# Performance work log

Measured on AMD Instinct MI355X. Metric: run time of the kernel, lower is better.

The kernel has to match this reference:

```python
import jax, jax.numpy as jnp
import numpy as np

D_MODEL = 768
CODEBOOK_SIZE = 2048
CODEBOOK_DIM = 64


def setup_inputs() -> dict:
    key = jax.random.key(0)
    ks = jax.random.split(key, 10)
    B, N = 16, 4096
    h = CODEBOOK_DIM * 2  # 128
    def lin_init(k, fan_in, shape):
        bound = 1.0 / np.sqrt(fan_in)
        return jax.random.uniform(k, shape, jnp.float32, -bound, bound)
    inp = {
        "x": jax.random.normal(ks[0], (B, N, D_MODEL), jnp.float32),
        # encoder: Linear(d_model -> 2*cd), GELU, Linear(2*cd -> cd)
        "enc_w1": lin_init(ks[1], D_MODEL, (D_MODEL, h)),
        "enc_b1": lin_init(ks[2], D_MODEL, (h,)),
        "enc_w2": lin_init(ks[3], h, (h, CODEBOOK_DIM)),
        "enc_b2": lin_init(ks[4], h, (CODEBOOK_DIM,)),
        # codebook: uniform(-1/K, 1/K)
        "codebook": jax.random.uniform(ks[5], (CODEBOOK_SIZE, CODEBOOK_DIM), jnp.float32,
                                        -1.0 / CODEBOOK_SIZE, 1.0 / CODEBOOK_SIZE),
        # decoder: Linear(cd -> 2*cd), GELU, Linear(2*cd -> d_model)
        "dec_w1": lin_init(ks[6], CODEBOOK_DIM, (CODEBOOK_DIM, h)),
        "dec_b1": lin_init(ks[7], CODEBOOK_DIM, (h,)),
        "dec_w2": lin_init(ks[8], h, (h, D_MODEL)),
        "dec_b2": lin_init(ks[9], h, (D_MODEL,)),
    }
    return inp


def reference(x, enc_w1, enc_b1, enc_w2, enc_b2, codebook, dec_w1, dec_b1, dec_w2, dec_b2):
    B, N, _ = x.shape
    # encoder MLP (exact GELU, matching torch default)
    z = jax.nn.gelu(x @ enc_w1 + enc_b1, approximate=False) @ enc_w2 + enc_b2  # (B,N,cd)
    # quantize: squared-distance argmin over codebook
    flat_z = z.reshape(-1, CODEBOOK_DIM)  # (BN, cd)
    dist = (jnp.sum(flat_z * flat_z, axis=1, keepdims=True)
            + jnp.sum(codebook * codebook, axis=1)[None, :]
            - 2.0 * flat_z @ codebook.T)  # (BN, K)
    indices = jnp.argmin(dist, axis=-1)  # (BN,)
    z_q = codebook[indices].reshape(B, N, CODEBOOK_DIM)
    codebook_loss = jnp.mean((jax.lax.stop_gradient(z_q) - z) ** 2)
    embedding_loss = jnp.mean((z_q - jax.lax.stop_gradient(z)) ** 2)
    vq_loss = codebook_loss + 0.25 * embedding_loss
    # straight-through estimator
    z_q = z + jax.lax.stop_gradient(z_q - z)
    # decoder MLP
    x_rec = jax.nn.gelu(z_q @ dec_w1 + dec_b1, approximate=False) @ dec_w2 + dec_b2
    return x_rec, indices.reshape(B, N), vq_loss
```

## Files before the change

### kernel.cpp

```cpp
#include <hip/hip_runtime.h>
#include <math.h>

#define TOKENS 65536
#define DMODEL 768
#define HDIM 128
#define CDIM 64
#define NCODE 2048

__device__ __forceinline__ float gelu_exact(float v) {
    return 0.5f * v * (1.0f + erff(v * 0.7071067811865476f));
}

__global__ __launch_bounds__(256)
void enc_fused(const float* __restrict__ x, const float* __restrict__ w1,
               const float* __restrict__ b1, const float* __restrict__ w2,
               const float* __restrict__ b2, float* __restrict__ Z)
{
    __shared__ union {
        struct { float Xs[64][32]; float Ws[32][128]; } pa;
        struct { float W2s[128][64]; } pb;
    } u;
    __shared__ float H1s[64][132];

    const int t = threadIdx.x;
    const size_t tok0 = (size_t)blockIdx.x * 64;

    const int tg = t >> 5;
    const int cg = t & 31;

    float acc[8][4];
    #pragma unroll
    for (int i = 0; i < 8; ++i)
        #pragma unroll
        for (int j = 0; j < 4; ++j) acc[i][j] = 0.f;

    const int ltok = t >> 2, lkg = t & 3;

    float4 xr0, xr1, wr[4];
    {
        const float4* src = reinterpret_cast<const float4*>(
            x + (tok0 + ltok) * DMODEL + lkg * 8);
        xr0 = src[0]; xr1 = src[1];
        #pragma unroll
        for (int i = 0; i < 4; ++i) {
            int f = t + i * 256;
            int row = f >> 5, c4 = f & 31;
            wr[i] = *reinterpret_cast<const float4*>(w1 + (size_t)row * HDIM + c4 * 4);
        }
    }

    for (int k0 = 0; k0 < DMODEL; k0 += 32) {
        {
            float4* dst = reinterpret_cast<float4*>(&u.pa.Xs[ltok][lkg * 8]);
            dst[0] = xr0; dst[1] = xr1;
            #pragma unroll
            for (int i = 0; i < 4; ++i) {
                int f = t + i * 256;
                int row = f >> 5, c4 = f & 31;
                *reinterpret_cast<float4*>(&u.pa.Ws[row][c4 * 4]) = wr[i];
            }
        }
        __syncthreads();
        if (k0 + 32 < DMODEL) {
            const float4* src = reinterpret_cast<const float4*>(
                x + (tok0 + ltok) * DMODEL + (k0 + 32) + lkg * 8);
            xr0 = src[0]; xr1 = src[1];
            #pragma unroll
            for (int i = 0; i < 4; ++i) {
                int f = t + i * 256;
                int row = f >> 5, c4 = f & 31;
                wr[i] = *reinterpret_cast<const float4*>(
                    w1 + (size_t)(k0 + 32 + row) * HDIM + c4 * 4);
            }
        }
        #pragma unroll
        for (int kk = 0; kk < 32; kk += 4) {
            float4 av[8];
            #pragma unroll
            for (int i = 0; i < 8; ++i)
                av[i] = *reinterpret_cast<const float4*>(&u.pa.Xs[tg * 8 + i][kk]);
            float4 bv[4];
            #pragma unroll
            for (int q = 0; q < 4; ++q)
                bv[q] = *reinterpret_cast<const float4*>(&u.pa.Ws[kk + q][cg * 4]);
            #pragma unroll
            for (int i = 0; i < 8; ++i) {
                acc[i][0] = fmaf(av[i].x, bv[0].x, acc[i][0]);
                acc[i][1] = fmaf(av[i].x, bv[0].y, acc[i][1]);
                acc[i][2] = fmaf(av[i].x, bv[0].z, acc[i][2]);
                acc[i][3] = fmaf(av[i].x, bv[0].w, acc[i][3]);
                acc[i][0] = fmaf(av[i].y, bv[1].x, acc[i][0]);
                acc[i][1] = fmaf(av[i].y, bv[1].y, acc[i][1]);
                acc[i][2] = fmaf(av[i].y, bv[1].z, acc[i][2]);
                acc[i][3] = fmaf(av[i].y, bv[1].w, acc[i][3]);
                acc[i][0] = fmaf(av[i].z, bv[2].x, acc[i][0]);
                acc[i][1] = fmaf(av[i].z, bv[2].y, acc[i][1]);
                acc[i][2] = fmaf(av[i].z, bv[2].z, acc[i][2]);
                acc[i][3] = fmaf(av[i].z, bv[2].w, acc[i][3]);
                acc[i][0] = fmaf(av[i].w, bv[3].x, acc[i][0]);
                acc[i][1] = fmaf(av[i].w, bv[3].y, acc[i][1]);
                acc[i][2] = fmaf(av[i].w, bv[3].z, acc[i][2]);
                acc[i][3] = fmaf(av[i].w, bv[3].w, acc[i][3]);
            }
        }
        __syncthreads();
    }
    {
        float4 b1v = *reinterpret_cast<const float4*>(b1 + cg * 4);
        #pragma unroll
        for (int i = 0; i < 8; ++i) {
            float4 h;
            h.x = gelu_exact(acc[i][0] + b1v.x);
            h.y = gelu_exact(acc[i][1] + b1v.y);
            h.z = gelu_exact(acc[i][2] + b1v.z);
            h.w = gelu_exact(acc[i][3] + b1v.w);
            *reinterpret_cast<float4*>(&H1s[tg * 8 + i][cg * 4]) = h;
        }
    }
    #pragma unroll
    for (int i = 0; i < 8; ++i) {
        int f = t + i * 256;
        int row = f >> 4, c4 = f & 15;
        *reinterpret_cast<float4*>(&u.pb.W2s[row][c4 * 4]) =
            *reinterpret_cast<const float4*>(w2 + (size_t)row * CDIM + c4 * 4);
    }
    __syncthreads();
    const int tg2 = t >> 4;
    const int cg2 = t & 15;
    float accB[4][4];
    #pragma unroll
    for (int i = 0; i < 4; ++i)
        #pragma unroll
        for (int j = 0; j < 4; ++j) accB[i][j] = 0.f;
    #pragma unroll
    for (int k = 0; k < HDIM; k += 4) {
        float4 av[4];
        #pragma unroll
        for (int i = 0; i < 4; ++i)
            av[i] = *reinterpret_cast<const float4*>(&H1s[tg2 * 4 + i][k]);
        float4 bv[4];
        #pragma unroll
        for (int q = 0; q < 4; ++q)
            bv[q] = *reinterpret_cast<const float4*>(&u.pb.W2s[k + q][cg2 * 4]);
        #pragma unroll
        for (int i = 0; i < 4; ++i) {
            accB[i][0] = fmaf(av[i].x, bv[0].x, accB[i][0]);
            accB[i][1] = fmaf(av[i].x, bv[0].y, accB[i][1]);
            accB[i][2] = fmaf(av[i].x, bv[0].z, accB[i][2]);
            accB[i][3] = fmaf(av[i].x, bv[0].w, accB[i][3]);
            accB[i][0] = fmaf(av[i].y, bv[1].x, accB[i][0]);
            accB[i][1] = fmaf(av[i].y, bv[1].y, accB[i][1]);
            accB[i][2] = fmaf(av[i].y, bv[1].z, accB[i][2]);
            accB[i][3] = fmaf(av[i].y, bv[1].w, accB[i][3]);
            accB[i][0] = fmaf(av[i].z, bv[2].x, accB[i][0]);
            accB[i][1] = fmaf(av[i].z, bv[2].y, accB[i][1]);
            accB[i][2] = fmaf(av[i].z, bv[2].z, accB[i][2]);
            accB[i][3] = fmaf(av[i].z, bv[2].w, accB[i][3]);
            accB[i][0] = fmaf(av[i].w, bv[3].x, accB[i][0]);
            accB[i][1] = fmaf(av[i].w, bv[3].y, accB[i][1]);
            accB[i][2] = fmaf(av[i].w, bv[3].z, accB[i][2]);
            accB[i][3] = fmaf(av[i].w, bv[3].w, accB[i][3]);
        }
    }
    {
        float4 b2v = *reinterpret_cast<const float4*>(b2 + cg2 * 4);
        #pragma unroll
        for (int i = 0; i < 4; ++i) {
            float4 o;
            o.x = accB[i][0] + b2v.x;
            o.y = accB[i][1] + b2v.y;
            o.z = accB[i][2] + b2v.z;
            o.w = accB[i][3] + b2v.w;
            *reinterpret_cast<float4*>(Z + (tok0 + tg2 * 4 + i) * CDIM + cg2 * 4) = o;
        }
    }
}

__global__ __launch_bounds__(256)
void vq_kernel(const float* __restrict__ Z, const float* __restrict__ cb,
               const float* __restrict__ cnorm, int* __restrict__ idx_out,
               float* __restrict__ idxf_out, float* __restrict__ loss_accum)
{
    __shared__ float Zs[64][64];
    __shared__ float CsT[64][128];
    __shared__ float tgsum[8];

    const int t = threadIdx.x;
    const size_t tok0 = (size_t)blockIdx.x * 64;
    const int tg = t >> 5, cg = t & 31;
    const int lc = t >> 1, lh = t & 1;

    {
        int ltok = t >> 2, lq = t & 3;
        const float4* src = reinterpret_cast<const float4*>(Z + (tok0 + ltok) * CDIM + lq * 16);
        float4* dst = reinterpret_cast<float4*>(&Zs[ltok][lq * 16]);
        dst[0] = src[0]; dst[1] = src[1]; dst[2] = src[2]; dst[3] = src[3];
    }
    float4 cv[8];
    {
        const float4* src = reinterpret_cast<const float4*>(cb + (size_t)lc * CDIM + lh * 32);
        #pragma unroll
        for (int i = 0; i < 8; ++i) cv[i] = src[i];
    }
    __syncthreads();

    float zn[8];
    {
        #pragma unroll
        for (int i = 0; i < 8; ++i) {
            float a = Zs[tg * 8 + i][cg * 2];
            float b = Zs[tg * 8 + i][cg * 2 + 1];
            zn[i] = fmaf(a, a, b * b);
        }
        #pragma unroll
        for (int m = 16; m >= 1; m >>= 1)
            #pragma unroll
            for (int i = 0; i < 8; ++i) zn[i] += __shfl_xor(zn[i], m, 32);
    }

    float minv[8]; int mini[8];
    #pragma unroll
    for (int i = 0; i < 8; ++i) { minv[i] = INFINITY; mini[i] = 0; }

    for (int tile = 0; tile < 16; ++tile) {
        const int code0 = tile * 128;
        __syncthreads();
        #pragma unroll
        for (int i = 0; i < 8; ++i) {
            int k = lh * 32 + i * 4;
            CsT[k + 0][lc] = cv[i].x;
            CsT[k + 1][lc] = cv[i].y;
            CsT[k + 2][lc] = cv[i].z;
            CsT[k + 3][lc] = cv[i].w;
        }
        __syncthreads();
        if (tile + 1 < 16) {
            const float4* src = reinterpret_cast<const float4*>(
                cb + (size_t)(code0 + 128 + lc) * CDIM + lh * 32);
            #pragma unroll
            for (int i = 0; i < 8; ++i) cv[i] = src[i];
        }

        float dot[8][4];
        #pragma unroll
        for (int i = 0; i < 8; ++i)
            #pragma unroll
            for (int j = 0; j < 4; ++j) dot[i][j] = 0.f;

        #pragma unroll
        for (int k = 0; k < CDIM; k += 4) {
            float4 av[8];
            #pragma unroll
            for (int i = 0; i < 8; ++i)
                av[i] = *reinterpret_cast<const float4*>(&Zs[tg * 8 + i][k]);
            float4 bv[4];
            #pragma unroll
            for (int q = 0; q < 4; ++q)
                bv[q] = *reinterpret_cast<const float4*>(&CsT[k + q][cg * 4]);
            #pragma unroll
            for (int i = 0; i < 8; ++i) {
                dot[i][0] = fmaf(av[i].x, bv[0].x, dot[i][0]);
                dot[i][1] = fmaf(av[i].x, bv[0].y, dot[i][1]);
                dot[i][2] = fmaf(av[i].x, bv[0].z, dot[i][2]);
                dot[i][3] = fmaf(av[i].x, bv[0].w, dot[i][3]);
                dot[i][0] = fmaf(av[i].y, bv[1].x, dot[i][0]);
                dot[i][1] = fmaf(av[i].y, bv[1].y, dot[i][1]);
                dot[i][2] = fmaf(av[i].y, bv[1].z, dot[i][2]);
                dot[i][3] = fmaf(av[i].y, bv[1].w, dot[i][3]);
                dot[i][0] = fmaf(av[i].z, bv[2].x, dot[i][0]);
                dot[i][1] = fmaf(av[i].z, bv[2].y, dot[i][1]);
                dot[i][2] = fmaf(av[i].z, bv[2].z, dot[i][2]);
                dot[i][3] = fmaf(av[i].z, bv[2].w, dot[i][3]);
                dot[i][0] = fmaf(av[i].w, bv[3].x, dot[i][0]);
                dot[i][1] = fmaf(av[i].w, bv[3].y, dot[i][1]);
                dot[i][2] = fmaf(av[i].w, bv[3].z, dot[i][2]);
                dot[i][3] = fmaf(av[i].w, bv[3].w, dot[i][3]);
            }
        }
        #pragma unroll
        for (int j = 0; j < 4; ++j) {
            int ci = code0 + cg * 4 + j;
            float cn = cnorm[ci];
            #pragma unroll
            for (int i = 0; i < 8; ++i) {
                float s = (zn[i] + cn) - 2.f * dot[i][j];
                if (s < minv[i]) { minv[i] = s; mini[i] = ci; }
            }
        }
    }

    #pragma unroll
    for (int i = 0; i < 8; ++i) {
        float v = minv[i]; int ci = mini[i];
        #pragma unroll
        for (int m = 16; m >= 1; m >>= 1) {
            float ov = __shfl_xor(v, m, 32);
            int oi = __shfl_xor(ci, m, 32);
            if (ov < v || (ov == v && oi < ci)) { v = ov; ci = oi; }
        }
        minv[i] = v; mini[i] = ci;
    }

    if (cg == 0) {
        float s = 0.f;
        #pragma unroll
        for (int i = 0; i < 8; ++i) {
            size_t tok = tok0 + tg * 8 + i;
            idx_out[tok] = mini[i];
            idxf_out[tok] = (float)mini[i];
            s += minv[i];
        }
        tgsum[tg] = s;
    }
    __syncthreads();
    if (t == 0) {
        float s = 0.f;
        #pragma unroll
        for (int i = 0; i < 8; ++i) s += tgsum[i];
        atomicAdd(loss_accum, s);
    }
}

__global__ __launch_bounds__(256)
void dec1_kernel(const float* __restrict__ cb, const float* __restrict__ w1,
                 const float* __restrict__ b1, float* __restrict__ T1,
                 float* __restrict__ cnorm)
{
    __shared__ float Cs[64][64];
    __shared__ float Ws[64][128];

    const int t = threadIdx.x;
    const int c0 = blockIdx.x * 64;
    {
        int lc = t >> 2, lq = t & 3;
        const float4* src = reinterpret_cast<const float4*>(cb + (size_t)(c0 + lc) * CDIM + lq * 16);
        float4* dst = reinterpret_cast<float4*>(&Cs[lc][lq * 16]);
        dst[0] = src[0]; dst[1] = src[1]; dst[2] = src[2]; dst[3] = src[3];
    }
    #pragma unroll
    for (int i = 0; i < 8; ++i) {
        int f = t + i * 256;
        int row = f >> 5, c4 = f & 31;
        *reinterpret_cast<float4*>(&Ws[row][c4 * 4]) =
            *reinterpret_cast<const float4*>(w1 + (size_t)row * HDIM + c4 * 4);
    }
    if (t < 64) {
        const float4* p = reinterpret_cast<const float4*>(cb + (size_t)(c0 + t) * CDIM);
        float s = 0.f;
        #pragma unroll
        for (int i = 0; i < 16; ++i) {
            float4 v = p[i];
            s = fmaf(v.x, v.x, s); s = fmaf(v.y, v.y, s);
            s = fmaf(v.z, v.z, s); s = fmaf(v.w, v.w, s);
        }
        cnorm[c0 + t] = s;
    }
    __syncthreads();
    const int tg = t >> 5, cg = t & 31;
    float acc[8][4];
    #pragma unroll
    for (int i = 0; i < 8; ++i)
        #pragma unroll
        for (int j = 0; j < 4; ++j) acc[i][j] = 0.f;
    #pragma unroll
    for (int k = 0; k < CDIM; k += 4) {
        float4 av[8];
        #pragma unroll
        for (int i = 0; i < 8; ++i)
            av[i] = *reinterpret_cast<const float4*>(&Cs[tg * 8 + i][k]);
        float4 bv[4];
        #pragma unroll
        for (int q = 0; q < 4; ++q)
            bv[q] = *reinterpret_cast<const float4*>(&Ws[k + q][cg * 4]);
        #pragma unroll
        for (int i = 0; i < 8; ++i) {
            acc[i][0] = fmaf(av[i].x, bv[0].x, acc[i][0]);
            acc[i][1] = fmaf(av[i].x, bv[0].y, acc[i][1]);
            acc[i][2] = fmaf(av[i].x, bv[0].z, acc[i][2]);
            acc[i][3] = fmaf(av[i].x, bv[0].w, acc[i][3]);
            acc[i][0] = fmaf(av[i].y, bv[1].x, acc[i][0]);
            acc[i][1] = fmaf(av[i].y, bv[1].y, acc[i][1]);
            acc[i][2] = fmaf(av[i].y, bv[1].z, acc[i][2]);
            acc[i][3] = fmaf(av[i].y, bv[1].w, acc[i][3]);
            acc[i][0] = fmaf(av[i].z, bv[2].x, acc[i][0]);
            acc[i][1] = fmaf(av[i].z, bv[2].y, acc[i][1]);
            acc[i][2] = fmaf(av[i].z, bv[2].z, acc[i][2]);
            acc[i][3] = fmaf(av[i].z, bv[2].w, acc[i][3]);
            acc[i][0] = fmaf(av[i].w, bv[3].x, acc[i][0]);
            acc[i][1] = fmaf(av[i].w, bv[3].y, acc[i][1]);
            acc[i][2] = fmaf(av[i].w, bv[3].z, acc[i][2]);
            acc[i][3] = fmaf(av[i].w, bv[3].w, acc[i][3]);
        }
    }
    float4 b1v = *reinterpret_cast<const float4*>(b1 + cg * 4);
    #pragma unroll
    for (int i = 0; i < 8; ++i) {
        float4 h;
        h.x = gelu_exact(acc[i][0] + b1v.x);
        h.y = gelu_exact(acc[i][1] + b1v.y);
        h.z = gelu_exact(acc[i][2] + b1v.z);
        h.w = gelu_exact(acc[i][3] + b1v.w);
        *reinterpret_cast<float4*>(T1 + (size_t)(c0 + tg * 8 + i) * HDIM + cg * 4) = h;
    }
}

__global__ __launch_bounds__(256)
void dec2_kernel(const float* __restrict__ T1, const float* __restrict__ w2,
                 const float* __restrict__ b2, float* __restrict__ table)
{
    __shared__ float As[64][32];
    __shared__ float Ws[32][128];
    const int t = threadIdx.x;
    const int r0 = blockIdx.x * 64;
    const int col0 = blockIdx.y * 128;
    const int tg = t >> 5, cg = t & 31;
    float acc[8][4];
    #pragma unroll
    for (int i = 0; i < 8; ++i)
        #pragma unroll
        for (int j = 0; j < 4; ++j) acc[i][j] = 0.f;

    for (int k0 = 0; k0 < HDIM; k0 += 32) {
        __syncthreads();
        {
            int lr = t >> 2, lk = t & 3;
            const float4* src = reinterpret_cast<const float4*>(T1 + (size_t)(r0 + lr) * HDIM + k0 + lk * 8);
            float4 v0 = src[0], v1 = src[1];
            float4* dst = reinterpret_cast<float4*>(&As[lr][lk * 8]);
            dst[0] = v0; dst[1] = v1;
        }
        #pragma unroll
        for (int i = 0; i < 4; ++i) {
            int f = t + i * 256;
            int row = f >> 5, c4 = f & 31;
            *reinterpret_cast<float4*>(&Ws[row][c4 * 4]) =
                *reinterpret_cast<const float4*>(w2 + (size_t)(k0 + row) * DMODEL + col0 + c4 * 4);
        }
        __syncthreads();
        #pragma unroll
        for (int kk = 0; kk < 32; kk += 4) {
            float4 av[8];
            #pragma unroll
            for (int i = 0; i < 8; ++i)
                av[i] = *reinterpret_cast<const float4*>(&As[tg * 8 + i][kk]);
            float4 bv[4];
            #pragma unroll
            for (int q = 0; q < 4; ++q)
                bv[q] = *reinterpret_cast<const float4*>(&Ws[kk + q][cg * 4]);
            #pragma unroll
            for (int i = 0; i < 8; ++i) {
                acc[i][0] = fmaf(av[i].x, bv[0].x, acc[i][0]);
                acc[i][1] = fmaf(av[i].x, bv[0].y, acc[i][1]);
                acc[i][2] = fmaf(av[i].x, bv[0].z, acc[i][2]);
                acc[i][3] = fmaf(av[i].x, bv[0].w, acc[i][3]);
                acc[i][0] = fmaf(av[i].y, bv[1].x, acc[i][0]);
                acc[i][1] = fmaf(av[i].y, bv[1].y, acc[i][1]);
                acc[i][2] = fmaf(av[i].y, bv[1].z, acc[i][2]);
                acc[i][3] = fmaf(av[i].y, bv[1].w, acc[i][3]);
                acc[i][0] = fmaf(av[i].z, bv[2].x, acc[i][0]);
                acc[i][1] = fmaf(av[i].z, bv[2].y, acc[i][1]);
                acc[i][2] = fmaf(av[i].z, bv[2].z, acc[i][2]);
                acc[i][3] = fmaf(av[i].z, bv[2].w, acc[i][3]);
                acc[i][0] = fmaf(av[i].w, bv[3].x, acc[i][0]);
                acc[i][1] = fmaf(av[i].w, bv[3].y, acc[i][1]);
                acc[i][2] = fmaf(av[i].w, bv[3].z, acc[i][2]);
                acc[i][3] = fmaf(av[i].w, bv[3].w, acc[i][3]);
            }
        }
    }
    float4 b2v = *reinterpret_cast<const float4*>(b2 + col0 + cg * 4);
    #pragma unroll
    for (int i = 0; i < 8; ++i) {
        float4 o;
        o.x = acc[i][0] + b2v.x;
        o.y = acc[i][1] + b2v.y;
        o.z = acc[i][2] + b2v.z;
        o.w = acc[i][3] + b2v.w;
        *reinterpret_cast<float4*>(table + (size_t)(r0 + tg * 8 + i) * DMODEL + col0 + cg * 4) = o;
    }
}

__global__ void gather_kernel(const float* __restrict__ table,
                              const int* __restrict__ idx, float* __restrict__ out,
                              const float* __restrict__ loss_accum,
                              float* __restrict__ loss_out)
{
    if (blockIdx.x == 0 && threadIdx.x == 0) {
        loss_out[0] = loss_accum[0] * (1.25f / 4194304.0f);
    }
    const int F = TOKENS * (DMODEL / 4);
    const float4* tab4 = reinterpret_cast<const float4*>(table);
    float4* out4 = reinterpret_cast<float4*>(out);
    for (int f = blockIdx.x * blockDim.x + threadIdx.x; f < F;
         f += gridDim.x * blockDim.x) {
        int token = f / 192;
        int j = f - token * 192;
        out4[f] = tab4[(size_t)idx[token] * 192 + j];
    }
}

extern "C" void kernel_launch(void* const* d_in, const int* in_sizes, int n_in,
                              void* d_out, int out_size, void* d_ws, size_t ws_size,
                              hipStream_t stream)
{
    const float* x      = (const float*)d_in[0];
    const float* enc_w1 = (const float*)d_in[1];
    const float* enc_b1 = (const float*)d_in[2];
    const float* enc_w2 = (const float*)d_in[3];
    const float* enc_b2 = (const float*)d_in[4];
    const float* cb     = (const float*)d_in[5];
    const float* dec_w1 = (const float*)d_in[6];
    const float* dec_b1 = (const float*)d_in[7];
    const float* dec_w2 = (const float*)d_in[8];
    const float* dec_b2 = (const float*)d_in[9];

    float* out     = (float*)d_out;
    float* xrec    = out;
    float* idxf    = out + (size_t)TOKENS * DMODEL;
    float* lossout = idxf + TOKENS;

    float* ws    = (float*)d_ws;
    float* Z     = ws;
    float* T1    = Z + (size_t)TOKENS * CDIM;
    float* table = T1 + (size_t)NCODE * HDIM;
    float* cnorm = table + (size_t)NCODE * DMODEL;
    int*   idx   = (int*)(cnorm + NCODE);
    float* lacc  = (float*)(idx + TOKENS);

    hipMemsetAsync(lacc, 0, sizeof(float), stream);

    enc_fused<<<TOKENS / 64, 256, 0, stream>>>(x, enc_w1, enc_b1, enc_w2, enc_b2, Z);
    dec1_kernel<<<NCODE / 64, 256, 0, stream>>>(cb, dec_w1, dec_b1, T1, cnorm);
    dec2_kernel<<<dim3(NCODE / 64, DMODEL / 128), 256, 0, stream>>>(T1, dec_w2, dec_b2, table);
    vq_kernel<<<TOKENS / 64, 256, 0, stream>>>(Z, cb, cnorm, idx, idxf, lacc);
    gather_kernel<<<2048, 256, 0, stream>>>(table, idx, xrec, lacc, lossout);
}
```

Before: 949.3 us.

## Pad shared tiles, interleave row mapping, and cut encoder LDS footprint

Shared-memory tiles across the encoder, VQ, and decoder kernels are padded (row strides 36/68) and thread-to-row mapping changes from contiguous (tg*8+i) to strided (tg+8*i), to reduce LDS bank conflicts on the float4 A-operand reads. The encoder's second GEMM now reads w2 directly from global memory with register double-buffering instead of staging it in LDS. H1s is folded into the union, shrinking LDS use, and launch_bounds asks for 4 blocks per CU to raise occupancy. The risks are extra global/L2 traffic for w2 and register pressure from the occupancy hint.

New measurement: 928.4 us. 1.02x faster.

```diff
diff --git a/kernel.cpp b/kernel.cpp
--- a/kernel.cpp
+++ b/kernel.cpp
@@ -11,20 +11,18 @@
     return 0.5f * v * (1.0f + erff(v * 0.7071067811865476f));
 }
 
-__global__ __launch_bounds__(256)
+__global__ __launch_bounds__(256, 4)
 void enc_fused(const float* __restrict__ x, const float* __restrict__ w1,
                const float* __restrict__ b1, const float* __restrict__ w2,
                const float* __restrict__ b2, float* __restrict__ Z)
 {
     __shared__ union {
-        struct { float Xs[64][32]; float Ws[32][128]; } pa;
-        struct { float W2s[128][64]; } pb;
+        struct { float Xs[64][36]; float Ws[32][128]; } a;
+        float H1s[64][132];
     } u;
-    __shared__ float H1s[64][132];
 
     const int t = threadIdx.x;
     const size_t tok0 = (size_t)blockIdx.x * 64;
-
     const int tg = t >> 5;
     const int cg = t & 31;
 
@@ -35,11 +33,11 @@
         for (int j = 0; j < 4; ++j) acc[i][j] = 0.f;
 
     const int ltok = t >> 2, lkg = t & 3;
+    const float* xrow = x + (tok0 + ltok) * DMODEL + lkg * 8;
 
     float4 xr0, xr1, wr[4];
     {
-        const float4* src = reinterpret_cast<const float4*>(
-            x + (tok0 + ltok) * DMODEL + lkg * 8);
+        const float4* src = reinterpret_cast<const float4*>(xrow);
         xr0 = src[0]; xr1 = src[1];
         #pragma unroll
         for (int i = 0; i < 4; ++i) {
@@ -51,19 +49,18 @@
 
     for (int k0 = 0; k0 < DMODEL; k0 += 32) {
         {
-            float4* dst = reinterpret_cast<float4*>(&u.pa.Xs[ltok][lkg * 8]);
+            float4* dst = reinterpret_cast<float4*>(&u.a.Xs[ltok][lkg * 8]);
             dst[0] = xr0; dst[1] = xr1;
             #pragma unroll
             for (int i = 0; i < 4; ++i) {
                 int f = t + i * 256;
                 int row = f >> 5, c4 = f & 31;
-                *reinterpret_cast<float4*>(&u.pa.Ws[row][c4 * 4]) = wr[i];
+                *reinterpret_cast<float4*>(&u.a.Ws[row][c4 * 4]) = wr[i];
             }
         }
         __syncthreads();
         if (k0 + 32 < DMODEL) {
-            const float4* src = reinterpret_cast<const float4*>(
-                x + (tok0 + ltok) * DMODEL + (k0 + 32) + lkg * 8);
+            const float4* src = reinterpret_cast<const float4*>(xrow + k0 + 32);
             xr0 = src[0]; xr1 = src[1];
             #pragma unroll
             for (int i = 0; i < 4; ++i) {
@@ -78,11 +75,11 @@
             float4 av[8];
             #pragma unroll
             for (int i = 0; i < 8; ++i)
-                av[i] = *reinterpret_cast<const float4*>(&u.pa.Xs[tg * 8 + i][kk]);
+                av[i] = *reinterpret_cast<const float4*>(&u.a.Xs[tg + 8 * i][kk]);
             float4 bv[4];
             #pragma unroll
             for (int q = 0; q < 4; ++q)
-                bv[q] = *reinterpret_cast<const float4*>(&u.pa.Ws[kk + q][cg * 4]);
+                bv[q] = *reinterpret_cast<const float4*>(&u.a.Ws[kk + q][cg * 4]);
             #pragma unroll
             for (int i = 0; i < 8; ++i) {
                 acc[i][0] = fmaf(av[i].x, bv[0].x, acc[i][0]);
@@ -105,6 +102,7 @@
         }
         __syncthreads();
     }
+
     {
         float4 b1v = *reinterpret_cast<const float4*>(b1 + cg * 4);
         #pragma unroll
@@ -114,34 +112,37 @@
             h.y = gelu_exact(acc[i][1] + b1v.y);
             h.z = gelu_exact(acc[i][2] + b1v.z);
             h.w = gelu_exact(acc[i][3] + b1v.w);
-            *reinterpret_cast<float4*>(&H1s[tg * 8 + i][cg * 4]) = h;
-        }
-    }
-    #pragma unroll
-    for (int i = 0; i < 8; ++i) {
-        int f = t + i * 256;
-        int row = f >> 4, c4 = f & 15;
-        *reinterpret_cast<float4*>(&u.pb.W2s[row][c4 * 4]) =
-            *reinterpret_cast<const float4*>(w2 + (size_t)row * CDIM + c4 * 4);
+            *reinterpret_cast<float4*>(&u.H1s[tg + 8 * i][cg * 4]) = h;
+        }
     }
     __syncthreads();
+
     const int tg2 = t >> 4;
     const int cg2 = t & 15;
+    const float4* w2_4 = reinterpret_cast<const float4*>(w2);
     float accB[4][4];
     #pragma unroll
     for (int i = 0; i < 4; ++i)
         #pragma unroll
         for (int j = 0; j < 4; ++j) accB[i][j] = 0.f;
-    #pragma unroll
+
+    float4 bvn[4];
+    #pragma unroll
+    for (int q = 0; q < 4; ++q) bvn[q] = w2_4[(size_t)q * 16 + cg2];
+
     for (int k = 0; k < HDIM; k += 4) {
+        float4 bv[4];
+        #pragma unroll
+        for (int q = 0; q < 4; ++q) bv[q] = bvn[q];
+        if (k + 4 < HDIM) {
+            #pragma unroll
+            for (int q = 0; q < 4; ++q)
+                bvn[q] = w2_4[(size_t)(k + 4 + q) * 16 + cg2];
+        }
         float4 av[4];
         #pragma unroll
         for (int i = 0; i < 4; ++i)
-            av[i] = *reinterpret_cast<const float4*>(&H1s[tg2 * 4 + i][k]);
-        float4 bv[4];
-        #pragma unroll
-        for (int q = 0; q < 4; ++q)
-            bv[q] = *reinterpret_cast<const float4*>(&u.pb.W2s[k + q][cg2 * 4]);
+            av[i] = *reinterpret_cast<const float4*>(&u.H1s[tg2 + 16 * i][k]);
         #pragma unroll
         for (int i = 0; i < 4; ++i) {
             accB[i][0] = fmaf(av[i].x, bv[0].x, accB[i][0]);
@@ -171,7 +172,7 @@
             o.y = accB[i][1] + b2v.y;
             o.z = accB[i][2] + b2v.z;
             o.w = accB[i][3] + b2v.w;
-            *reinterpret_cast<float4*>(Z + (tok0 + tg2 * 4 + i) * CDIM + cg2 * 4) = o;
+            *reinterpret_cast<float4*>(Z + (tok0 + tg2 + 16 * i) * CDIM + cg2 * 4) = o;
         }
     }
 }
@@ -181,7 +182,7 @@
                const float* __restrict__ cnorm, int* __restrict__ idx_out,
                float* __restrict__ idxf_out, float* __restrict__ loss_accum)
 {
-    __shared__ float Zs[64][64];
+    __shared__ float Zs[64][68];
     __shared__ float CsT[64][128];
     __shared__ float tgsum[8];
 
@@ -208,8 +209,8 @@
     {
         #pragma unroll
         for (int i = 0; i < 8; ++i) {
-            float a = Zs[tg * 8 + i][cg * 2];
-            float b = Zs[tg * 8 + i][cg * 2 + 1];
+            float a = Zs[tg + 8 * i][cg * 2];
+            float b = Zs[tg + 8 * i][cg * 2 + 1];
             zn[i] = fmaf(a, a, b * b);
         }
         #pragma unroll
@@ -252,7 +253,7 @@
             float4 av[8];
             #pragma unroll
             for (int i = 0; i < 8; ++i)
-                av[i] = *reinterpret_cast<const float4*>(&Zs[tg * 8 + i][k]);
+                av[i] = *reinterpret_cast<const float4*>(&Zs[tg + 8 * i][k]);
             float4 bv[4];
             #pragma unroll
             for (int q = 0; q < 4; ++q)
@@ -305,7 +306,7 @@
         float s = 0.f;
         #pragma unroll
         for (int i = 0; i < 8; ++i) {
-            size_t tok = tok0 + tg * 8 + i;
+            size_t tok = tok0 + tg + 8 * i;
             idx_out[tok] = mini[i];
             idxf_out[tok] = (float)mini[i];
             s += minv[i];
@@ -326,7 +327,7 @@
                  const float* __restrict__ b1, float* __restrict__ T1,
                  float* __restrict__ cnorm)
 {
-    __shared__ float Cs[64][64];
+    __shared__ float Cs[64][68];
     __shared__ float Ws[64][128];
 
     const int t = threadIdx.x;
@@ -367,7 +368,7 @@
         float4 av[8];
         #pragma unroll
         for (int i = 0; i < 8; ++i)
-            av[i] = *reinterpret_cast<const float4*>(&Cs[tg * 8 + i][k]);
+            av[i] = *reinterpret_cast<const float4*>(&Cs[tg + 8 * i][k]);
         float4 bv[4];
         #pragma unroll
         for (int q = 0; q < 4; ++q)
@@ -400,7 +401,7 @@
         h.y = gelu_exact(acc[i][1] + b1v.y);
         h.z = gelu_exact(acc[i][2] + b1v.z);
         h.w = gelu_exact(acc[i][3] + b1v.w);
-        *reinterpret_cast<float4*>(T1 + (size_t)(c0 + tg * 8 + i) * HDIM + cg * 4) = h;
+        *reinterpret_cast<float4*>(T1 + (size_t)(c0 + tg + 8 * i) * HDIM + cg * 4) = h;
     }
 }
 
@@ -408,7 +409,7 @@
 void dec2_kernel(const float* __restrict__ T1, const float* __restrict__ w2,
                  const float* __restrict__ b2, float* __restrict__ table)
 {
-    __shared__ float As[64][32];
+    __shared__ float As[64][36];
     __shared__ float Ws[32][128];
     const int t = threadIdx.x;
     const int r0 = blockIdx.x * 64;
@@ -442,7 +443,7 @@
             float4 av[8];
             #pragma unroll
             for (int i = 0; i < 8; ++i)
-                av[i] = *reinterpret_cast<const float4*>(&As[tg * 8 + i][kk]);
+                av[i] = *reinterpret_cast<const float4*>(&As[tg + 8 * i][kk]);
             float4 bv[4];
             #pragma unroll
             for (int q = 0; q < 4; ++q)
@@ -476,7 +477,7 @@
         o.y = acc[i][1] + b2v.y;
         o.z = acc[i][2] + b2v.z;
         o.w = acc[i][3] + b2v.w;
-        *reinterpret_cast<float4*>(table + (size_t)(r0 + tg * 8 + i) * DMODEL + col0 + cg * 4) = o;
+        *reinterpret_cast<float4*>(table + (size_t)(r0 + tg + 8 * i) * DMODEL + col0 + cg * 4) = o;
     }
 }
 
```
